# Kernel tuning notes

Hardware: AMD Instinct MI355X
Metric: run time of the kernel (lower is better)

Reference implementation:

```python
import jax, jax.numpy as jnp
import numpy as np


def setup_inputs() -> dict:
    key = jax.random.key(0)
    k1, k2, k3, k4, k5 = jax.random.split(key, 5)
    B, T, H, E, F = 4, 2048, 2048, 8, 1024
    s_h = 1.0 / np.sqrt(H)
    s_f = 1.0 / np.sqrt(F)
    return {
        "hidden_states": jax.random.normal(k1, (B, T, H), dtype=jnp.float32),
        "W_router": jax.random.normal(k2, (H, E), dtype=jnp.float32) * s_h,
        "W_gate": jax.random.normal(k3, (E, H, F), dtype=jnp.float32) * s_h,
        "W_up": jax.random.normal(k4, (E, H, F), dtype=jnp.float32) * s_h,
        "W_down": jax.random.normal(k5, (E, F, H), dtype=jnp.float32) * s_f,
    }


def reference(hidden_states, W_router, W_gate, W_up, W_down):
    B, T, H = hidden_states.shape
    E = W_router.shape[1]
    x = hidden_states.reshape(-1, H)  # [N, H]
    # ReMoE router: linear -> ReLU, non-negative weights per expert
    weights = jax.nn.relu(x @ W_router)  # [N, E]
    # Per-expert SwiGLU FFN applied to all tokens; zero-weight experts
    # contribute exactly zero, matching the original masked dispatch.
    gate = jnp.einsum('nh,ehf->enf', x, W_gate)  # [E, N, F]
    up = jnp.einsum('nh,ehf->enf', x, W_up)      # [E, N, F]
    hid = jax.nn.silu(gate) * up                 # [E, N, F]
    expert_out = jnp.einsum('enf,efh->enh', hid, W_down)  # [E, N, H]
    out_flat = jnp.einsum('ne,enh->nh', weights, expert_out)  # [N, H]
    out = out_flat.reshape(B, T, H)
    router_weights = weights.reshape(B, T, E)
    return (out, router_weights)
```

## Files before the change

kernel.cpp:

```cpp
#include <hip/hip_runtime.h>
#include <hip/hip_bf16.h>

#define N_TOK 8192
#define HD    2048
#define NE    8
#define FF    1024

using f32x4  = __attribute__((ext_vector_type(4))) float;
using bf16x8 = __attribute__((ext_vector_type(8))) __bf16;

__device__ __forceinline__ unsigned short f2bf(float f) {
  unsigned u = __float_as_uint(f);
  u += 0x7FFFu + ((u >> 16) & 1u);
  return (unsigned short)(u >> 16);
}

__device__ __forceinline__ void gl_lds16(const void* g, void* l) {
  __builtin_amdgcn_global_load_lds((__attribute__((address_space(1))) void*)g,
                                   (__attribute__((address_space(3))) void*)l,
                                   16, 0, 0);
}

__device__ __forceinline__ void stage256(const unsigned short* g, size_t lda, int k0,
                                         char* slotbase, int wv, int sr8, int scol) {
  #pragma unroll
  for (int c = 0; c < 4; ++c) {
    const int grp = c * 8 + wv;
    gl_lds16(g + (size_t)(grp * 8 + sr8) * lda + k0 + scol, slotbase + grp * 1024);
  }
}
__device__ __forceinline__ void stage256i(const unsigned short* const aP[4], int k0,
                                          char* slotbase, int wv) {
  #pragma unroll
  for (int c = 0; c < 4; ++c) {
    const int grp = c * 8 + wv;
    gl_lds16(aP[c] + k0, slotbase + grp * 1024);
  }
}
__device__ __forceinline__ void stage128(const unsigned short* g, size_t lda, int k0,
                                         char* slotbase, int wv, int sr8, int scol) {
  #pragma unroll
  for (int c = 0; c < 2; ++c) {
    const int grp = c * 8 + wv;
    gl_lds16(g + (size_t)(grp * 8 + sr8) * lda + k0 + scol, slotbase + grp * 1024);
  }
}
__device__ __forceinline__ void stage64(const unsigned short* g, size_t lda, int k0,
                                        char* slotbase, int wv, int sr8, int scol) {
  gl_lds16(g + (size_t)(wv * 8 + sr8) * lda + k0 + scol, slotbase + wv * 1024);
}

__global__ void k_tconv(const float* __restrict__ in, unsigned short* __restrict__ out,
                        int R, int C, size_t in_z, size_t out_z, size_t ostride) {
  __shared__ float tile[32][33];
  const int z = blockIdx.z;
  const int c0 = blockIdx.x * 32, r0 = blockIdx.y * 32;
  const int tx = threadIdx.x, ty = threadIdx.y;
  const float* ip = in + (size_t)z * in_z;
  unsigned short* op = out + (size_t)z * out_z;
  #pragma unroll
  for (int i = ty; i < 32; i += 8)
    tile[i][tx] = ip[(size_t)(r0 + i) * C + (c0 + tx)];
  __syncthreads();
  #pragma unroll
  for (int i = ty; i < 32; i += 8)
    op[(size_t)(c0 + i) * ostride + (r0 + tx)] = f2bf(tile[tx][i]);
}

__global__ void k_router(const float* __restrict__ x, const float* __restrict__ Wr,
                         float* __restrict__ w, float* __restrict__ rout,
                         unsigned short* __restrict__ xb) {
  const int lane = threadIdx.x & 63, wv = threadIdx.x >> 6;
  const int n = blockIdx.x * 4 + wv;
  const float* xr = x + (size_t)n * HD + lane * 32;
  unsigned short* xbr = xb + (size_t)n * HD + lane * 32;
  const float* wbase = Wr + (size_t)lane * 32 * NE;
  float acc[8];
  #pragma unroll
  for (int e = 0; e < 8; ++e) acc[e] = 0.f;
  #pragma unroll
  for (int kk = 0; kk < 32; kk += 4) {
    float4 xv = *reinterpret_cast<const float4*>(xr + kk);
    ushort4 o;
    o.x = f2bf(xv.x); o.y = f2bf(xv.y); o.z = f2bf(xv.z); o.w = f2bf(xv.w);
    *reinterpret_cast<ushort4*>(xbr + kk) = o;
    #pragma unroll
    for (int t = 0; t < 4; ++t) {
      const float* wrow = wbase + (kk + t) * 8;
      float4 w0 = *reinterpret_cast<const float4*>(wrow);
      float4 w1 = *reinterpret_cast<const float4*>(wrow + 4);
      float xs = (t == 0) ? xv.x : (t == 1) ? xv.y : (t == 2) ? xv.z : xv.w;
      acc[0] += xs * w0.x; acc[1] += xs * w0.y; acc[2] += xs * w0.z; acc[3] += xs * w0.w;
      acc[4] += xs * w1.x; acc[5] += xs * w1.y; acc[6] += xs * w1.z; acc[7] += xs * w1.w;
    }
  }
  #pragma unroll
  for (int off = 32; off; off >>= 1) {
    #pragma unroll
    for (int e = 0; e < 8; ++e) acc[e] += __shfl_down(acc[e], off);
  }
  if (lane == 0) {
    #pragma unroll
    for (int e = 0; e < 8; ++e) {
      float v = acc[e] > 0.f ? acc[e] : 0.f;
      w[n * 8 + e] = v;
      rout[n * 8 + e] = v;
    }
  }
}

__global__ void k_compact(const float* __restrict__ w, int* __restrict__ idx,
                          int* __restrict__ cnt) {
  const int e = blockIdx.x;
  __shared__ int base;
  __shared__ int scan[4];
  if (threadIdx.x == 0) base = 0;
  __syncthreads();
  const int lane = threadIdx.x & 63, wvi = threadIdx.x >> 6;
  for (int c0 = 0; c0 < N_TOK; c0 += 256) {
    const int n = c0 + threadIdx.x;
    const bool act = w[n * 8 + e] > 0.f;
    unsigned long long m = __ballot(act);
    const int pre  = __popcll(m & ((1ull << lane) - 1ull));
    if (lane == 0) scan[wvi] = __popcll(m);
    __syncthreads();
    int woff = 0;
    #pragma unroll
    for (int i = 0; i < 4; ++i) if (i < wvi) woff += scan[i];
    const int tot = scan[0] + scan[1] + scan[2] + scan[3];
    if (act) idx[e * N_TOK + base + woff + pre] = n;
    __syncthreads();
    if (threadIdx.x == 0) base += tot;
    __syncthreads();
  }
  const int M = base;
  if (threadIdx.x == 0) cnt[e] = M;
  const int Mpad = (M + 255) & ~255;
  for (int i = M + threadIdx.x; i < Mpad; i += 256) idx[e * N_TOK + i] = 0;
}

#define G1_PHASE(mq) do {                                                        \
    const char* Ab_ = As + sA * 32768 + (wr * 128 + (mq) * 64) * 128 + rb;       \
    const char* Bg_ = Bgs + sBr * 8192 + (wc * 16) * 128 + rb;                   \
    const char* Bu_ = Bus + sBr * 8192 + (wc * 16) * 128 + rb;                   \
    bf16x8 av_[4][2];                                                            \
    _Pragma("unroll")                                                            \
    for (int i = 0; i < 4; ++i) {                                                \
      av_[i][0] = *(const bf16x8*)(Ab_ + i * 2048 + cp0);                        \
      av_[i][1] = *(const bf16x8*)(Ab_ + i * 2048 + cp1);                        \
    }                                                                            \
    bf16x8 bg0_ = *(const bf16x8*)(Bg_ + cp0);                                   \
    bf16x8 bg1_ = *(const bf16x8*)(Bg_ + cp1);                                   \
    bf16x8 bu0_ = *(const bf16x8*)(Bu_ + cp0);                                   \
    bf16x8 bu1_ = *(const bf16x8*)(Bu_ + cp1);                                   \
    __builtin_amdgcn_s_setprio(1);                                               \
    _Pragma("unroll")                                                            \
    for (int i = 0; i < 4; ++i) {                                                \
      ag[(mq)*4+i] = __builtin_amdgcn_mfma_f32_16x16x32_bf16(av_[i][0], bg0_, ag[(mq)*4+i], 0,0,0); \
      au[(mq)*4+i] = __builtin_amdgcn_mfma_f32_16x16x32_bf16(av_[i][0], bu0_, au[(mq)*4+i], 0,0,0); \
      ag[(mq)*4+i] = __builtin_amdgcn_mfma_f32_16x16x32_bf16(av_[i][1], bg1_, ag[(mq)*4+i], 0,0,0); \
      au[(mq)*4+i] = __builtin_amdgcn_mfma_f32_16x16x32_bf16(av_[i][1], bu1_, au[(mq)*4+i], 0,0,0); \
    }                                                                            \
    __builtin_amdgcn_s_setprio(0);                                               \
  } while (0)

__global__ void __launch_bounds__(512, 2) k_gemm1(
    const unsigned short* __restrict__ xb,
    const unsigned short* __restrict__ Wg,
    const unsigned short* __restrict__ Wu,
    const float* __restrict__ w,
    const int* __restrict__ idx,
    const int* __restrict__ cnt,
    unsigned short* __restrict__ A2,
    int e0, int k2g, int nwg) {
  extern __shared__ char lds[];
  char* As  = lds;
  char* Bgs = lds + 98304;
  char* Bus = lds + 114688;
  const int tid = threadIdx.x;
  const int l = tid & 63, wv = tid >> 6;

  const int h = blockIdx.x;
  const int chunk = nwg >> 3;
  const int L = (h & 7) * chunk + (h >> 3);
  const int eloc = L >> 9;
  const int e = e0 + eloc;
  const int idxq = L & 511;
  const int sub = idxq >> 5;
  const int f = ((sub & 3) << 2) | ((idxq >> 3) & 3);
  const int y = ((sub >> 2) << 3) | (idxq & 7);
  const int bm = y << 8;
  const int bf = f << 6;
  const int wr = wv >> 2, wc = wv & 3;

  const int Me = cnt[e];
  if (bm >= Me) return;
  const int* idxe = idx + e * N_TOK;

  const unsigned short* gBg = Wg + ((size_t)e * FF + bf) * HD;
  const unsigned short* gBu = Wu + ((size_t)e * FF + bf) * HD;

  const int sr8  = l >> 3;
  const int scol = ((l & 7) ^ sr8) << 3;
  const int fr  = l & 15;
  const int rb  = fr << 7;
  const int kc  = (l >> 4) << 4;
  const int swz = (l & 7) << 4;
  const int cp0 = kc ^ swz;
  const int cp1 = (64 + kc) ^ swz;

  const unsigned short* aP[4];
  #pragma unroll
  for (int c = 0; c < 4; ++c)
    aP[c] = xb + (size_t)idxe[bm + (c * 8 + wv) * 8 + sr8] * HD + scol;

  f32x4 ag[8], au[8];
  const f32x4 zero = {0.f, 0.f, 0.f, 0.f};
  #pragma unroll
  for (int i = 0; i < 8; ++i) { ag[i] = zero; au[i] = zero; }

  stage256i(aP, 0, As, wv);
  stage64(gBg, HD, 0, Bgs, wv, sr8, scol);
  stage64(gBu, HD, 0, Bus, wv, sr8, scol);
  stage256i(aP, 64, As + 32768, wv);
  asm volatile("s_waitcnt vmcnt(4)" ::: "memory");
  __builtin_amdgcn_s_barrier();
  __builtin_amdgcn_sched_barrier(0);

  const int NT = HD / 64;
  int sA = 0;
  for (int t = 0; t < NT; ++t) {
    const int tB = (t + 1 < NT) ? t + 1 : NT - 1;
    const int tA = (t + 2 < NT) ? t + 2 : NT - 1;
    const int sBw = (t + 1) & 1;
    const int sBr = t & 1;
    const int sAw = (sA >= 1) ? sA - 1 : 2;
    stage64(gBg, HD, tB * 64, Bgs + sBw * 8192, wv, sr8, scol);
    stage64(gBu, HD, tB * 64, Bus + sBw * 8192, wv, sr8, scol);
    G1_PHASE(0);
    stage256i(aP, tA * 64, As + sAw * 32768, wv);
    G1_PHASE(1);
    asm volatile("s_waitcnt vmcnt(4)" ::: "memory");
    __builtin_amdgcn_s_barrier();
    __builtin_amdgcn_sched_barrier(0);
    sA = (sA == 2) ? 0 : sA + 1;
  }

  const int orow = (l >> 4) << 2;
  #pragma unroll
  for (int am = 0; am < 8; ++am) {
    #pragma unroll
    for (int rr = 0; rr < 4; ++rr) {
      const int cm = bm + wr * 128 + am * 16 + orow + rr;
      const int n = idxe[cm];
      const float wn = w[n * 8 + e];
      const float g = ag[am][rr];
      const float u = au[am][rr];
      const float s = g / (1.f + __expf(-g));
      A2[(size_t)n * k2g + (size_t)eloc * FF + bf + wc * 16 + fr] = f2bf(s * u * wn);
    }
  }
}

#define G2_PHASE(mq) do {                                                        \
    const char* Ab_ = As + sA * 32768 + (wr * 128 + (mq) * 64) * 128 + rb;       \
    const char* Bb_ = Bs + sBr * 16384 + (wc * 32) * 128 + rb;                   \
    bf16x8 av_[4][2];                                                            \
    bf16x8 bv_[2][2];                                                            \
    _Pragma("unroll")                                                            \
    for (int i = 0; i < 4; ++i) {                                                \
      av_[i][0] = *(const bf16x8*)(Ab_ + i * 2048 + cp0);                        \
      av_[i][1] = *(const bf16x8*)(Ab_ + i * 2048 + cp1);                        \
    }                                                                            \
    _Pragma("unroll")                                                            \
    for (int j = 0; j < 2; ++j) {                                                \
      bv_[j][0] = *(const bf16x8*)(Bb_ + j * 2048 + cp0);                        \
      bv_[j][1] = *(const bf16x8*)(Bb_ + j * 2048 + cp1);                        \
    }                                                                            \
    __builtin_amdgcn_s_setprio(1);                                               \
    _Pragma("unroll")                                                            \
    for (int i = 0; i < 4; ++i) {                                                \
      _Pragma("unroll")                                                          \
      for (int j = 0; j < 2; ++j) {                                              \
        acc[(mq)*4+i][j] = __builtin_amdgcn_mfma_f32_16x16x32_bf16(av_[i][0], bv_[j][0], acc[(mq)*4+i][j], 0,0,0); \
        acc[(mq)*4+i][j] = __builtin_amdgcn_mfma_f32_16x16x32_bf16(av_[i][1], bv_[j][1], acc[(mq)*4+i][j], 0,0,0); \
      }                                                                          \
    }                                                                            \
    __builtin_amdgcn_s_setprio(0);                                               \
  } while (0)

__global__ void __launch_bounds__(512, 2) k_gemm2(
    const unsigned short* __restrict__ A2,
    const unsigned short* __restrict__ Wd,
    float* __restrict__ out,
    int k2g, int accum) {
  extern __shared__ char lds[];
  char* As = lds;
  char* Bs = lds + 98304;
  const int tid = threadIdx.x;
  const int l = tid & 63, wv = tid >> 6;

  const int h = blockIdx.x;
  const int L = (h & 7) * 64 + (h >> 3);
  const int y = L >> 4;
  const int x = L & 15;
  const int bm = y << 8;
  const int bn = x << 7;
  const int wr = wv >> 2, wc = wv & 3;

  const unsigned short* gA = A2 + (size_t)bm * k2g;
  const unsigned short* gB = Wd + (size_t)bn * (NE * FF);

  const int sr8  = l >> 3;
  const int scol = ((l & 7) ^ sr8) << 3;
  const int fr  = l & 15;
  const int rb  = fr << 7;
  const int kc  = (l >> 4) << 4;
  const int swz = (l & 7) << 4;
  const int cp0 = kc ^ swz;
  const int cp1 = (64 + kc) ^ swz;

  f32x4 acc[8][2];
  const f32x4 zero = {0.f, 0.f, 0.f, 0.f};
  #pragma unroll
  for (int i = 0; i < 8; ++i) { acc[i][0] = zero; acc[i][1] = zero; }

  stage256(gA, k2g, 0, As, wv, sr8, scol);
  stage128(gB, NE * FF, 0, Bs, wv, sr8, scol);
  stage256(gA, k2g, 64, As + 32768, wv, sr8, scol);
  asm volatile("s_waitcnt vmcnt(4)" ::: "memory");
  __builtin_amdgcn_s_barrier();
  __builtin_amdgcn_sched_barrier(0);

  const int NT = k2g / 64;
  int sA = 0;
  for (int t = 0; t < NT; ++t) {
    const int tB = (t + 1 < NT) ? t + 1 : NT - 1;
    const int tA = (t + 2 < NT) ? t + 2 : NT - 1;
    const int sBw = (t + 1) & 1;
    const int sBr = t & 1;
    const int sAw = (sA >= 1) ? sA - 1 : 2;
    stage128(gB, NE * FF, tB * 64, Bs + sBw * 16384, wv, sr8, scol);
    G2_PHASE(0);
    stage256(gA, k2g, tA * 64, As + sAw * 32768, wv, sr8, scol);
    G2_PHASE(1);
    asm volatile("s_waitcnt vmcnt(4)" ::: "memory");
    __builtin_amdgcn_s_barrier();
    __builtin_amdgcn_sched_barrier(0);
    sA = (sA == 2) ? 0 : sA + 1;
  }

  const int orow = (l >> 4) << 2;
  #pragma unroll
  for (int am = 0; am < 8; ++am) {
    #pragma unroll
    for (int rr = 0; rr < 4; ++rr) {
      const int n = bm + wr * 128 + am * 16 + orow + rr;
      float* op = out + (size_t)n * HD + bn + wc * 32 + fr;
      #pragma unroll
      for (int j = 0; j < 2; ++j) {
        const float v = acc[am][j][rr];
        op[j * 16] = accum ? (op[j * 16] + v) : v;
      }
    }
  }
}

extern "C" void kernel_launch(void* const* d_in, const int* in_sizes, int n_in,
                              void* d_out, int out_size, void* d_ws, size_t ws_size,
                              hipStream_t stream) {
  (void)in_sizes; (void)out_size;
  if (n_in < 5) return;
  const float* x  = (const float*)d_in[0];
  const float* Wr = (const float*)d_in[1];
  const float* Wg = (const float*)d_in[2];
  const float* Wu = (const float*)d_in[3];
  const float* Wd = (const float*)d_in[4];
  float* out  = (float*)d_out;
  float* rout = out + (size_t)N_TOK * HD;

  hipFuncSetAttribute((const void*)k_gemm1, hipFuncAttributeMaxDynamicSharedMemorySize, 131072);
  hipFuncSetAttribute((const void*)k_gemm2, hipFuncAttributeMaxDynamicSharedMemorySize, 131072);

  char* ws = (char*)d_ws;
  const size_t SZ_XB = (size_t)N_TOK * HD * 2;
  const size_t SZ_W  = (size_t)NE * HD * FF * 2;
  unsigned short* xb    = (unsigned short*)(ws);
  unsigned short* Wg_bt = (unsigned short*)(ws + SZ_XB);
  unsigned short* Wu_bt = (unsigned short*)(ws + SZ_XB + SZ_W);
  unsigned short* Wd_bt = (unsigned short*)(ws + SZ_XB + 2 * SZ_W);
  float*          wbuf  = (float*)(ws + SZ_XB + 3 * SZ_W);
  size_t off = SZ_XB + 3 * SZ_W + (size_t)N_TOK * NE * 4;
  int* idxbuf = (int*)(ws + off);  off += (size_t)NE * N_TOK * 4;
  int* cntbuf = (int*)(ws + off);  off += 256;
  const size_t fixed = off;
  unsigned short* A2 = (unsigned short*)(ws + fixed);

  const size_t perE = (size_t)N_TOK * FF * 2;
  int G = 8;
  while (G > 1 && fixed + (size_t)G * perE > ws_size) G >>= 1;

  dim3 tb(32, 8);
  k_tconv<<<dim3(FF / 32, HD / 32, NE), tb, 0, stream>>>(
      Wg, Wg_bt, HD, FF, (size_t)HD * FF, (size_t)FF * HD, (size_t)HD);
  k_tconv<<<dim3(FF / 32, HD / 32, NE), tb, 0, stream>>>(
      Wu, Wu_bt, HD, FF, (size_t)HD * FF, (size_t)FF * HD, (size_t)HD);
  k_tconv<<<dim3(HD / 32, FF / 32, NE), tb, 0, stream>>>(
      Wd, Wd_bt, FF, HD, (size_t)FF * HD, (size_t)FF, (size_t)(NE * FF));

  k_router<<<N_TOK / 4, 256, 0, stream>>>(x, Wr, wbuf, rout, xb);

  k_compact<<<NE, 256, 0, stream>>>(wbuf, idxbuf, cntbuf);

  const int k2g = G * FF;
  for (int e0 = 0; e0 < NE; e0 += G) {
    hipMemsetAsync(A2, 0, (size_t)G * perE, stream);
    const int nwg1 = 512 * G;
    k_gemm1<<<nwg1, 512, 131072, stream>>>(xb, Wg_bt, Wu_bt, wbuf, idxbuf, cntbuf,
                                           A2, e0, k2g, nwg1);
    k_gemm2<<<512, 512, 131072, stream>>>(A2, Wd_bt + (size_t)e0 * FF, out, k2g, e0 != 0);
  }
}
```

Measured before the change: 769.8 us.

## Make down-projection sparse per expert with compacted rows and atomic scatter

The first GEMM now writes its expert activations in compacted per-expert row order instead of scattering them into a dense token-by-(G*FF) buffer. The down-projection GEMM becomes per-expert over compacted rows and skips tiles beyond each expert's active token count. Its results are scattered to the output through the token index with float atomic adds into an output zeroed up front. This removes the A2 memset and the dense K=G*FF GEMM over all tokens, at the cost of atomic contention and nondeterministic summation order.

```diff
diff --git a/kernel.cpp b/kernel.cpp
--- a/kernel.cpp
+++ b/kernel.cpp
@@ -172,7 +172,7 @@
     const int* __restrict__ idx,
     const int* __restrict__ cnt,
     unsigned short* __restrict__ A2,
-    int e0, int k2g, int nwg) {
+    int e0, int nwg) {
   extern __shared__ char lds[];
   char* As  = lds;
   char* Bgs = lds + 98304;
@@ -246,6 +246,7 @@
     sA = (sA == 2) ? 0 : sA + 1;
   }
 
+  unsigned short* A2e = A2 + (size_t)eloc * N_TOK * FF;
   const int orow = (l >> 4) << 2;
   #pragma unroll
   for (int am = 0; am < 8; ++am) {
@@ -257,7 +258,7 @@
       const float g = ag[am][rr];
       const float u = au[am][rr];
       const float s = g / (1.f + __expf(-g));
-      A2[(size_t)n * k2g + (size_t)eloc * FF + bf + wc * 16 + fr] = f2bf(s * u * wn);
+      A2e[(size_t)cm * FF + bf + wc * 16 + fr] = f2bf(s * u * wn);
     }
   }
 }
@@ -292,8 +293,10 @@
 __global__ void __launch_bounds__(512, 2) k_gemm2(
     const unsigned short* __restrict__ A2,
     const unsigned short* __restrict__ Wd,
+    const int* __restrict__ idx,
+    const int* __restrict__ cnt,
     float* __restrict__ out,
-    int k2g, int accum) {
+    int e0, int nwg) {
   extern __shared__ char lds[];
   char* As = lds;
   char* Bs = lds + 98304;
@@ -301,15 +304,24 @@
   const int l = tid & 63, wv = tid >> 6;
 
   const int h = blockIdx.x;
-  const int L = (h & 7) * 64 + (h >> 3);
-  const int y = L >> 4;
-  const int x = L & 15;
+  const int chunk = nwg >> 3;
+  const int L = (h & 7) * chunk + (h >> 3);
+  const int eloc = L >> 9;
+  const int e = e0 + eloc;
+  const int idxq = L & 511;
+  const int sub = idxq >> 5;
+  const int x = ((sub & 3) << 2) | ((idxq >> 3) & 3);
+  const int y = ((sub >> 2) << 3) | (idxq & 7);
   const int bm = y << 8;
   const int bn = x << 7;
   const int wr = wv >> 2, wc = wv & 3;
 
-  const unsigned short* gA = A2 + (size_t)bm * k2g;
-  const unsigned short* gB = Wd + (size_t)bn * (NE * FF);
+  const int Me = cnt[e];
+  if (bm >= Me) return;
+  const int* idxe = idx + e * N_TOK;
+
+  const unsigned short* gA = A2 + (size_t)eloc * N_TOK * FF + (size_t)bm * FF;
+  const unsigned short* gB = Wd + (size_t)bn * (NE * FF) + (size_t)e * FF;
 
   const int sr8  = l >> 3;
   const int scol = ((l & 7) ^ sr8) << 3;
@@ -325,14 +337,14 @@
   #pragma unroll
   for (int i = 0; i < 8; ++i) { acc[i][0] = zero; acc[i][1] = zero; }
 
-  stage256(gA, k2g, 0, As, wv, sr8, scol);
+  stage256(gA, FF, 0, As, wv, sr8, scol);
   stage128(gB, NE * FF, 0, Bs, wv, sr8, scol);
-  stage256(gA, k2g, 64, As + 32768, wv, sr8, scol);
+  stage256(gA, FF, 64, As + 32768, wv, sr8, scol);
   asm volatile("s_waitcnt vmcnt(4)" ::: "memory");
   __builtin_amdgcn_s_barrier();
   __builtin_amdgcn_sched_barrier(0);
 
-  const int NT = k2g / 64;
+  const int NT = FF / 64;
   int sA = 0;
   for (int t = 0; t < NT; ++t) {
     const int tB = (t + 1 < NT) ? t + 1 : NT - 1;
@@ -342,7 +354,7 @@
     const int sAw = (sA >= 1) ? sA - 1 : 2;
     stage128(gB, NE * FF, tB * 64, Bs + sBw * 16384, wv, sr8, scol);
     G2_PHASE(0);
-    stage256(gA, k2g, tA * 64, As + sAw * 32768, wv, sr8, scol);
+    stage256(gA, FF, tA * 64, As + sAw * 32768, wv, sr8, scol);
     G2_PHASE(1);
     asm volatile("s_waitcnt vmcnt(4)" ::: "memory");
     __builtin_amdgcn_s_barrier();
@@ -355,12 +367,12 @@
   for (int am = 0; am < 8; ++am) {
     #pragma unroll
     for (int rr = 0; rr < 4; ++rr) {
-      const int n = bm + wr * 128 + am * 16 + orow + rr;
-      float* op = out + (size_t)n * HD + bn + wc * 32 + fr;
-      #pragma unroll
-      for (int j = 0; j < 2; ++j) {
-        const float v = acc[am][j][rr];
-        op[j * 16] = accum ? (op[j * 16] + v) : v;
+      const int cm = bm + wr * 128 + am * 16 + orow + rr;
+      if (cm < Me) {
+        const int n = idxe[cm];
+        float* op = out + (size_t)n * HD + bn + wc * 32 + fr;
+        unsafeAtomicAdd(op,      acc[am][0][rr]);
+        unsafeAtomicAdd(op + 16, acc[am][1][rr]);
       }
     }
   }
@@ -369,7 +381,7 @@
 extern "C" void kernel_launch(void* const* d_in, const int* in_sizes, int n_in,
                               void* d_out, int out_size, void* d_ws, size_t ws_size,
                               hipStream_t stream) {
-  (void)in_sizes; (void)out_size;
+  (void)in_sizes;
   if (n_in < 5) return;
   const float* x  = (const float*)d_in[0];
   const float* Wr = (const float*)d_in[1];
@@ -400,6 +412,8 @@
   int G = 8;
   while (G > 1 && fixed + (size_t)G * perE > ws_size) G >>= 1;
 
+  hipMemsetAsync(out, 0, (size_t)N_TOK * HD * 4, stream);
+
   dim3 tb(32, 8);
   k_tconv<<<dim3(FF / 32, HD / 32, NE), tb, 0, stream>>>(
       Wg, Wg_bt, HD, FF, (size_t)HD * FF, (size_t)FF * HD, (size_t)HD);
@@ -412,12 +426,10 @@
 
   k_compact<<<NE, 256, 0, stream>>>(wbuf, idxbuf, cntbuf);
 
-  const int k2g = G * FF;
   for (int e0 = 0; e0 < NE; e0 += G) {
-    hipMemsetAsync(A2, 0, (size_t)G * perE, stream);
-    const int nwg1 = 512 * G;
-    k_gemm1<<<nwg1, 512, 131072, stream>>>(xb, Wg_bt, Wu_bt, wbuf, idxbuf, cntbuf,
-                                           A2, e0, k2g, nwg1);
-    k_gemm2<<<512, 512, 131072, stream>>>(A2, Wd_bt + (size_t)e0 * FF, out, k2g, e0 != 0);
-  }
-}
+    const int nwg = 512 * G;
+    k_gemm1<<<nwg, 512, 131072, stream>>>(xb, Wg_bt, Wu_bt, wbuf, idxbuf, cntbuf,
+                                          A2, e0, nwg);
+    k_gemm2<<<nwg, 512, 131072, stream>>>(A2, Wd_bt, idxbuf, cntbuf, out, e0, nwg);
+  }
+}
```

Measured after the change: 928.6 us. +20.6%, slower.
